# Kernel optimization log

Measured on AMD Instinct MI355X. Metric: run time of the kernel, lower is better.

Reference implementation:

```python
import jax, jax.numpy as jnp
import numpy as np

B, C, H, W = 16, 512, 32, 32
NUM_HEADS = 8
GROUPS = 32
EPS = 1e-5


def setup_inputs() -> dict:
    key = jax.random.key(0)
    ks = jax.random.split(key, 3)
    x = jax.random.normal(ks[0], (B, C, H, W), dtype=jnp.float32)
    # Conv2d 1x1 weights stored as (out, in); init ~ fan-in scaled normal
    qkv_w = jax.random.normal(ks[1], (3 * C, C), dtype=jnp.float32) * (C ** -0.5)
    proj_w = jax.random.normal(ks[2], (C, C), dtype=jnp.float32) * (C ** -0.5)
    return {
        "x": x,
        "norm_w": jnp.ones((C,), jnp.float32),
        "norm_b": jnp.zeros((C,), jnp.float32),
        "qkv_w": qkv_w,
        "qkv_b": jnp.zeros((3 * C,), jnp.float32),
        "proj_w": proj_w,
        "proj_b": jnp.zeros((C,), jnp.float32),
    }


def reference(x, norm_w, norm_b, qkv_w, qkv_b, proj_w, proj_b):
    b, c, hh, ww = x.shape
    nh = NUM_HEADS
    hd = c // nh
    n = hh * ww

    # GroupNorm(32, C)
    xg = x.reshape(b, GROUPS, c // GROUPS, hh, ww)
    mean = xg.mean(axis=(2, 3, 4), keepdims=True)
    var = ((xg - mean) ** 2).mean(axis=(2, 3, 4), keepdims=True)
    hn = ((xg - mean) * jax.lax.rsqrt(var + EPS)).reshape(b, c, hh, ww)
    hn = hn * norm_w[None, :, None, None] + norm_b[None, :, None, None]

    # 1x1 conv QKV projection
    qkv = jnp.einsum('bchw,oc->bohw', hn, qkv_w) + qkv_b[None, :, None, None]
    # (B,3C,H,W) -> (B,3,nh,hd,N) -> (3,B,nh,N,hd)
    qkv = qkv.reshape(b, 3, nh, hd, n).transpose(1, 0, 2, 4, 3)
    q, k, v = qkv[0], qkv[1], qkv[2]

    scale = hd ** -0.5
    attn = jax.nn.softmax(jnp.einsum('bhnd,bhmd->bhnm', q, k) * scale, axis=-1)
    o = jnp.einsum('bhnm,bhmd->bhnd', attn, v)  # (B,nh,N,hd)
    o = o.transpose(0, 1, 3, 2).reshape(b, c, hh, ww)

    out = jnp.einsum('bchw,oc->bohw', o, proj_w) + proj_b[None, :, None, None]
    return out + x
```

## Files before the change

### kernel.cpp

```cpp
#include <hip/hip_runtime.h>
#include <cstdint>
#include <math.h>


typedef __bf16 bf16;
typedef __attribute__((ext_vector_type(8))) __bf16 bf16x8;
typedef __attribute__((ext_vector_type(4))) float f32x4;
typedef __attribute__((ext_vector_type(4))) short s16x4;

union U8 { uint4 u4; bf16x8 v; bf16 h[8]; };
union U4 { ushort4 u; bf16 h[4]; };
union UB4 { ushort4 u; s16x4 s; bf16 h[4]; };
union F4 { float4 v; float f[4]; };

typedef __attribute__((address_space(1))) void* gp1;
typedef __attribute__((address_space(3))) void* lp3;

__device__ __forceinline__ void async16(const void* g, void* l) {
  __builtin_amdgcn_global_load_lds((gp1)g, (lp3)l, 16, 0, 0);
}

#define LOG2E 1.44269504f

__global__ __launch_bounds__(256) void cvt_w(const float* __restrict__ qw,
                                             const float* __restrict__ pw,
                                             bf16* __restrict__ qwb,
                                             bf16* __restrict__ pwb) {
  int i = blockIdx.x * 256 + threadIdx.x;
  F4 v; bf16* dst;
  if (i < 196608) { v.v = ((const float4*)qw)[i]; dst = qwb + (size_t)i * 4; }
  else { v.v = ((const float4*)pw)[i - 196608]; dst = pwb + (size_t)(i - 196608) * 4; }
  U4 o;
#pragma unroll
  for (int j = 0; j < 4; j++) o.h[j] = (bf16)v.f[j];
  *(ushort4*)dst = o.u;
}

__global__ __launch_bounds__(256) void gn_stats(const float* __restrict__ x,
                                                float2* __restrict__ stats) {
  int bg = blockIdx.x;
  const float* base = x + (size_t)bg * 16384;
  int t = threadIdx.x;
  float s = 0.f, ss = 0.f;
#pragma unroll
  for (int p = 0; p < 16; p++) {
    F4 u; u.v = *(const float4*)(base + (size_t)(p * 256 + t) * 4);
#pragma unroll
    for (int i = 0; i < 4; i++) { float v = u.f[i]; s += v; ss += v * v; }
  }
  for (int off = 1; off < 64; off <<= 1) { s += __shfl_xor(s, off); ss += __shfl_xor(ss, off); }
  __shared__ float red[8];
  int w = t >> 6;
  if ((t & 63) == 0) { red[w] = s; red[4 + w] = ss; }
  __syncthreads();
  if (t == 0) {
    float S = red[0] + red[1] + red[2] + red[3];
    float SS = red[4] + red[5] + red[6] + red[7];
    float mean = S * (1.f / 16384.f);
    float var = SS * (1.f / 16384.f) - mean * mean;
    stats[bg] = make_float2(mean, rsqrtf(var + 1e-5f));
  }
}

__global__ __launch_bounds__(256) void gn_apply(const float* __restrict__ x,
                                                const float* __restrict__ nwp,
                                                const float* __restrict__ nbp,
                                                const float2* __restrict__ stats,
                                                bf16* __restrict__ hnt) {
  int b = blockIdx.z, nt = blockIdx.y, ct = blockIdx.x;
  int t = threadIdx.x, w = t >> 6, l = t & 63;
  int wc = w & 1, wn = w >> 1;
  int cb = ct * 128 + wc * 64 + (l & 7) * 8;
  int n0 = nt * 64 + wn * 32 + (l >> 3) * 4;
  float2 ms = stats[b * 32 + (cb >> 4)];
  float wgt[8], bia[8];
#pragma unroll
  for (int i = 0; i < 8; i++) {
    float wi = nwp[cb + i] * ms.y;
    wgt[i] = wi;
    bia[i] = nbp[cb + i] - ms.x * wi;
  }
  F4 in[8];
  const float* xb = x + ((size_t)b * 512 + cb) * 1024 + n0;
#pragma unroll
  for (int i = 0; i < 8; i++) in[i].v = *(const float4*)(xb + (size_t)i * 1024);
  bf16* ob = hnt + ((size_t)b * 1024 + n0) * 512 + cb;
#pragma unroll
  for (int j = 0; j < 4; j++) {
    U8 o;
#pragma unroll
    for (int i = 0; i < 8; i++) o.h[i] = (bf16)(in[i].f[j] * wgt[i] + bia[i]);
    *(uint4*)(ob + (size_t)j * 512) = o.u4;
  }
}

__device__ __forceinline__ void gemm_bt_core(const bf16* ga0, const bf16* gb0,
                                             bf16* At, bf16* Bt,
                                             f32x4 (&acc)[4][4], int w, int l) {
  const bf16* ga = ga0 + (size_t)(w * 16 + (l >> 2)) * 512 + (l & 3) * 8;
  const bf16* gb = gb0 + (size_t)(w * 16 + (l >> 2)) * 512 + (l & 3) * 8;
  int wr = w >> 1, wc = w & 1;
  const bf16* Ab = At + (wr * 64 + (l & 15)) * 32 + (l >> 4) * 8;
  const bf16* Bb = Bt + (wc * 64 + (l & 15)) * 32 + (l >> 4) * 8;
  bf16* lA = At + w * 16 * 32;
  bf16* lB = Bt + w * 16 * 32;
  for (int k0 = 0; k0 < 512; k0 += 32) {
    async16(ga + k0, lA);
    async16(ga + 64 * 512 + k0, lA + 64 * 32);
    async16(gb + k0, lB);
    async16(gb + 64 * 512 + k0, lB + 64 * 32);
    __syncthreads();
    bf16x8 af[4], bfr[4];
#pragma unroll
    for (int i = 0; i < 4; i++) {
      af[i] = *(const bf16x8*)(Ab + i * 512);
      bfr[i] = *(const bf16x8*)(Bb + i * 512);
    }
#pragma unroll
    for (int i = 0; i < 4; i++)
#pragma unroll
      for (int j = 0; j < 4; j++)
        acc[i][j] = __builtin_amdgcn_mfma_f32_16x16x32_bf16(af[i], bfr[j], acc[i][j], 0, 0, 0);
    __syncthreads();
  }
}

__global__ __launch_bounds__(256, 2) void qkv_gemm(const bf16* __restrict__ hnt,
                                                   const bf16* __restrict__ qwb,
                                                   const float* __restrict__ qb,
                                                   bf16* __restrict__ qsw,
                                                   bf16* __restrict__ ksw,
                                                   bf16* __restrict__ vsw) {
  __shared__ bf16 At[128 * 32];
  __shared__ bf16 Bt[128 * 32];
  int b = blockIdx.z, mt = blockIdx.y, ot = blockIdx.x;
  int m0 = mt * 128, o0 = ot * 128;
  int t = threadIdx.x, w = t >> 6, l = t & 63;
  f32x4 acc[4][4] = {};
  gemm_bt_core(hnt + ((size_t)b * 1024 + m0) * 512, qwb + (size_t)o0 * 512, At, Bt, acc, w, l);

  int wr = w >> 1, wc = w & 1, quad = l >> 4, li = l & 15;
#pragma unroll
  for (int i = 0; i < 4; i++) {
    int gnb = m0 + wr * 64 + i * 16;
    int blk = gnb >> 4;
#pragma unroll
    for (int j = 0; j < 4; j++) {
      int go = o0 + wc * 64 + j * 16 + li;
      float bias = qb[go];
      if (ot < 8) {
        int c = (ot < 4) ? go : (go - 512);
        int hh = c >> 6, d = c & 63;
        int ks = d >> 5, dq = (d >> 3) & 3, jj = d & 7;
        bf16* base = ((ot < 4) ? qsw : ksw) + ((size_t)(b * 8 + hh) << 16)
                     + (blk * 2 + ks) * 512 + dq * 8 + jj;
#pragma unroll
        for (int r = 0; r < 4; r++)
          base[(quad * 4 + r) * 32] = (bf16)(acc[i][j][r] + bias);
      } else {
        int c = go - 1024;
        int hh = c >> 6, d = c & 63;
        int df = d >> 4, lv = d & 15;
        bf16* base = vsw + ((size_t)(b * 8 + hh) << 16)
                     + (blk * 4 + df) * 256 + (lv * 4 + quad) * 4;
        U4 pk;
#pragma unroll
        for (int r = 0; r < 4; r++) pk.h[r] = (bf16)(acc[i][j][r] + bias);
        *(ushort4*)base = pk.u;
      }
    }
  }
}

__global__ __launch_bounds__(256, 4) void attn(const bf16* __restrict__ qsw,
                                               const bf16* __restrict__ ksw,
                                               const bf16* __restrict__ vsw,
                                               bf16* __restrict__ ont) {
  int bh = blockIdx.x;
  int b = bh >> 3, h = bh & 7;
  int qt = blockIdx.y;
  int t = threadIdx.x, w = t >> 6, l = t & 63;
  int quad = l >> 4, li = l & 15;
  int q0 = qt * 128 + w * 32;

  int laneK = (li * 4 + quad) * 8;
  int laneV = (li * 4 + quad) * 4;
  const bf16* qp = qsw + ((size_t)bh << 16) + laneK;
  const bf16* kp = ksw + ((size_t)bh << 16) + laneK;
  const bf16* vp = vsw + ((size_t)bh << 16) + laneV;

  const float QS = 0.125f * LOG2E;
  bf16x8 qfr[2][2];
#pragma unroll
  for (int qf = 0; qf < 2; qf++)
#pragma unroll
    for (int ks = 0; ks < 2; ks++) {
      U8 u;
      u.u4 = *(const uint4*)(qp + (((q0 >> 4) + qf) * 2 + ks) * 512);
#pragma unroll
      for (int i = 0; i < 8; i++) u.h[i] = (bf16)((float)u.h[i] * QS);
      qfr[qf][ks] = u.v;
    }

  float mrun[2] = {-INFINITY, -INFINITY}, lrun[2] = {0.f, 0.f};
  f32x4 of[4][2] = {};

  U8 ka[2], kc[2];
#pragma unroll
  for (int kf = 0; kf < 2; kf++) {
    ka[kf].u4 = *(const uint4*)(kp + kf * 1024);
    kc[kf].u4 = *(const uint4*)(kp + kf * 1024 + 512);
  }

  for (int c = 0; c < 32; c++) {
    int cb = c * 2048;
    UB4 va[2][4];
#pragma unroll
    for (int kf = 0; kf < 2; kf++)
#pragma unroll
      for (int df = 0; df < 4; df++)
        va[kf][df].u = *(const ushort4*)(vp + cb + kf * 1024 + df * 256);
    f32x4 st[2][2] = {};
#pragma unroll
    for (int kf = 0; kf < 2; kf++) {
      st[0][kf] = __builtin_amdgcn_mfma_f32_16x16x32_bf16(ka[kf].v, qfr[0][0], st[0][kf], 0, 0, 0);
      st[1][kf] = __builtin_amdgcn_mfma_f32_16x16x32_bf16(ka[kf].v, qfr[1][0], st[1][kf], 0, 0, 0);
      st[0][kf] = __builtin_amdgcn_mfma_f32_16x16x32_bf16(kc[kf].v, qfr[0][1], st[0][kf], 0, 0, 0);
      st[1][kf] = __builtin_amdgcn_mfma_f32_16x16x32_bf16(kc[kf].v, qfr[1][1], st[1][kf], 0, 0, 0);
    }
    int cn = ((c + 1) & 31) * 2048;
    U8 nka[2], nkc[2];
#pragma unroll
    for (int kf = 0; kf < 2; kf++) {
      nka[kf].u4 = *(const uint4*)(kp + cn + kf * 1024);
      nkc[kf].u4 = *(const uint4*)(kp + cn + kf * 1024 + 512);
    }
    UB4 pfr[2][2];
#pragma unroll
    for (int qf = 0; qf < 2; qf++) {
      f32x4 vm = st[qf][0];
#pragma unroll
      for (int r = 0; r < 4; r++) vm[r] = fmaxf(vm[r], st[qf][1][r]);
      float mt = fmaxf(fmaxf(vm[0], vm[1]), fmaxf(vm[2], vm[3]));
      mt = fmaxf(mt, __shfl_xor(mt, 16));
      mt = fmaxf(mt, __shfl_xor(mt, 32));
      float mold = mrun[qf];
      float mnew = fmaxf(mold, mt);
      mrun[qf] = mnew;
      f32x4 vs = {};
#pragma unroll
      for (int kf = 0; kf < 2; kf++)
#pragma unroll
        for (int r = 0; r < 4; r++) {
          float e = __builtin_amdgcn_exp2f(st[qf][kf][r] - mnew);
          vs[r] += e;
          pfr[qf][kf].h[r] = (bf16)e;
        }
      float ls = (vs[0] + vs[1]) + (vs[2] + vs[3]);
      ls += __shfl_xor(ls, 16);
      ls += __shfl_xor(ls, 32);
      if (__ballot(mnew > mold)) {
        float alpha = __builtin_amdgcn_exp2f(mold - mnew);
        lrun[qf] = lrun[qf] * alpha + ls;
#pragma unroll
        for (int df = 0; df < 4; df++)
#pragma unroll
          for (int r = 0; r < 4; r++) of[df][qf][r] *= alpha;
      } else {
        lrun[qf] += ls;
      }
    }
#pragma unroll
    for (int kf = 0; kf < 2; kf++)
#pragma unroll
      for (int df = 0; df < 4; df++)
#pragma unroll
        for (int qf = 0; qf < 2; qf++)
          of[df][qf] = __builtin_amdgcn_mfma_f32_16x16x16bf16_1k(va[kf][df].s, pfr[qf][kf].s, of[df][qf], 0, 0, 0);
#pragma unroll
    for (int kf = 0; kf < 2; kf++) { ka[kf] = nka[kf]; kc[kf] = nkc[kf]; }
  }
#pragma unroll
  for (int qf = 0; qf < 2; qf++) {
    float inv = 1.f / lrun[qf];
    bf16* ob = ont + ((size_t)b * 1024 + q0 + qf * 16 + li) * 512 + h * 64 + quad * 4;
#pragma unroll
    for (int df = 0; df < 4; df++) {
      U4 pk;
#pragma unroll
      for (int r = 0; r < 4; r++) pk.h[r] = (bf16)(of[df][qf][r] * inv);
      *(ushort4*)(ob + df * 16) = pk.u;
    }
  }
}

__global__ __launch_bounds__(256, 2) void proj_gemm(const bf16* __restrict__ ont,
                                                    const bf16* __restrict__ pwb,
                                                    const float* __restrict__ pb,
                                                    const float* __restrict__ x,
                                                    float* __restrict__ out) {
  __shared__ bf16 At[128 * 32];
  __shared__ bf16 Bt[128 * 32];
  int b = blockIdx.z, mt = blockIdx.y, ot = blockIdx.x;
  int m0 = mt * 128, o0 = ot * 128;
  int t = threadIdx.x, w = t >> 6, l = t & 63;
  f32x4 acc[4][4] = {};
  gemm_bt_core(ont + ((size_t)b * 1024 + m0) * 512, pwb + (size_t)o0 * 512, At, Bt, acc, w, l);

  int wr = w >> 1, wc = w & 1, quad = l >> 4, li = l & 15;
#pragma unroll
  for (int i = 0; i < 4; i++) {
    int gn = m0 + wr * 64 + i * 16 + quad * 4;
#pragma unroll
    for (int j = 0; j < 4; j++) {
      int go = o0 + wc * 64 + j * 16 + li;
      float bias = pb[go];
      F4 xres; xres.v = *(const float4*)(x + ((size_t)b * 512 + go) * 1024 + gn);
      F4 o;
#pragma unroll
      for (int r = 0; r < 4; r++) o.f[r] = acc[i][j][r] + bias + xres.f[r];
      *(float4*)(out + ((size_t)b * 512 + go) * 1024 + gn) = o.v;
    }
  }
}

extern "C" void kernel_launch(void* const* d_in, const int* in_sizes, int n_in,
                              void* d_out, int out_size, void* d_ws, size_t ws_size,
                              hipStream_t stream) {
  const float* x  = (const float*)d_in[0];
  const float* nw = (const float*)d_in[1];
  const float* nb = (const float*)d_in[2];
  const float* qw = (const float*)d_in[3];
  const float* qb = (const float*)d_in[4];
  const float* pw = (const float*)d_in[5];
  const float* pb = (const float*)d_in[6];
  float* out = (float*)d_out;

  char* ws = (char*)d_ws;
  float2* stats = (float2*)ws;
  bf16* qwb = (bf16*)(ws + (64u << 10));
  bf16* pwb = (bf16*)(ws + (2u << 20));
  bf16* hnt = (bf16*)(ws + (4u << 20));
  bf16* qsw = (bf16*)(ws + (20u << 20));
  bf16* ksw = (bf16*)(ws + (36u << 20));
  bf16* vsw = (bf16*)(ws + (52u << 20));
  bf16* ont = hnt;

  cvt_w<<<1024, 256, 0, stream>>>(qw, pw, qwb, pwb);
  gn_stats<<<512, 256, 0, stream>>>(x, stats);
  gn_apply<<<dim3(4, 16, 16), 256, 0, stream>>>(x, nw, nb, stats, hnt);
  qkv_gemm<<<dim3(12, 8, 16), 256, 0, stream>>>(hnt, qwb, qb, qsw, ksw, vsw);
  attn<<<dim3(128, 8, 1), 256, 0, stream>>>(qsw, ksw, vsw, ont);
  proj_gemm<<<dim3(4, 8, 16), 256, 0, stream>>>(ont, pwb, pb, x, out);
}
```

Measured before the change: 231.2 us.

## Use lazy max rescaling and deferred row-sum reduction in attention loop

The attention inner loop now rescales the running max only when a tile's max exceeds the current max by more than 8 (in log2 units), skipping the cross-lane max shuffles otherwise. Row sums are kept as per-lane partial vectors and reduced across lanes once at the end instead of every iteration. The loop is manually unrolled by two with ping-pong K register buffers, removing the copies, and s_setprio raises wave priority around the MFMA blocks. The lazy threshold lets exp2 values reach up to 2^8 before rescaling, which relies on fp32 and bf16 range to stay accurate.

Measured after the change: 238.3 us. 3.1% more time.

```diff
diff --git a/kernel.cpp b/kernel.cpp
--- a/kernel.cpp
+++ b/kernel.cpp
@@ -172,6 +172,77 @@
   }
 }
 
+__device__ __forceinline__ void attn_body(const bf16* __restrict__ kp,
+                                          const bf16* __restrict__ vp, int c,
+                                          U8 (&ka)[2], U8 (&kc)[2],
+                                          U8 (&nka)[2], U8 (&nkc)[2],
+                                          const bf16x8 (&qfr)[2][2],
+                                          float (&mrun)[2], f32x4 (&lacc)[2],
+                                          f32x4 (&of)[4][2]) {
+  int cb = c * 2048;
+  UB4 va[2][4];
+#pragma unroll
+  for (int kf = 0; kf < 2; kf++)
+#pragma unroll
+    for (int df = 0; df < 4; df++)
+      va[kf][df].u = *(const ushort4*)(vp + cb + kf * 1024 + df * 256);
+  f32x4 st[2][2] = {};
+  __builtin_amdgcn_s_setprio(1);
+#pragma unroll
+  for (int kf = 0; kf < 2; kf++) {
+    st[0][kf] = __builtin_amdgcn_mfma_f32_16x16x32_bf16(ka[kf].v, qfr[0][0], st[0][kf], 0, 0, 0);
+    st[1][kf] = __builtin_amdgcn_mfma_f32_16x16x32_bf16(ka[kf].v, qfr[1][0], st[1][kf], 0, 0, 0);
+    st[0][kf] = __builtin_amdgcn_mfma_f32_16x16x32_bf16(kc[kf].v, qfr[0][1], st[0][kf], 0, 0, 0);
+    st[1][kf] = __builtin_amdgcn_mfma_f32_16x16x32_bf16(kc[kf].v, qfr[1][1], st[1][kf], 0, 0, 0);
+  }
+  __builtin_amdgcn_s_setprio(0);
+  int cn = ((c + 1) & 31) * 2048;
+#pragma unroll
+  for (int kf = 0; kf < 2; kf++) {
+    nka[kf].u4 = *(const uint4*)(kp + cn + kf * 1024);
+    nkc[kf].u4 = *(const uint4*)(kp + cn + kf * 1024 + 512);
+  }
+  UB4 pfr[2][2];
+#pragma unroll
+  for (int qf = 0; qf < 2; qf++) {
+    float mt = fmaxf(fmaxf(fmaxf(st[qf][0][0], st[qf][0][1]),
+                           fmaxf(st[qf][0][2], st[qf][0][3])),
+                     fmaxf(fmaxf(st[qf][1][0], st[qf][1][1]),
+                           fmaxf(st[qf][1][2], st[qf][1][3])));
+    if (__ballot(mt > mrun[qf] + 8.f)) {
+      mt = fmaxf(mt, __shfl_xor(mt, 16));
+      mt = fmaxf(mt, __shfl_xor(mt, 32));
+      float mnew = fmaxf(mrun[qf], mt);
+      float alpha = __builtin_amdgcn_exp2f(mrun[qf] - mnew);
+      mrun[qf] = mnew;
+#pragma unroll
+      for (int r = 0; r < 4; r++) lacc[qf][r] *= alpha;
+#pragma unroll
+      for (int df = 0; df < 4; df++)
+#pragma unroll
+        for (int r = 0; r < 4; r++) of[df][qf][r] *= alpha;
+    }
+    float m = mrun[qf];
+#pragma unroll
+    for (int kf = 0; kf < 2; kf++)
+#pragma unroll
+      for (int r = 0; r < 4; r++) {
+        float e = __builtin_amdgcn_exp2f(st[qf][kf][r] - m);
+        lacc[qf][r] += e;
+        pfr[qf][kf].h[r] = (bf16)e;
+      }
+  }
+  __builtin_amdgcn_s_setprio(1);
+#pragma unroll
+  for (int kf = 0; kf < 2; kf++)
+#pragma unroll
+    for (int df = 0; df < 4; df++)
+#pragma unroll
+      for (int qf = 0; qf < 2; qf++)
+        of[df][qf] = __builtin_amdgcn_mfma_f32_16x16x16bf16_1k(va[kf][df].s, pfr[qf][kf].s, of[df][qf], 0, 0, 0);
+  __builtin_amdgcn_s_setprio(0);
+}
+
 __global__ __launch_bounds__(256, 4) void attn(const bf16* __restrict__ qsw,
                                                const bf16* __restrict__ ksw,
                                                const bf16* __restrict__ vsw,
@@ -202,87 +273,28 @@
       qfr[qf][ks] = u.v;
     }
 
-  float mrun[2] = {-INFINITY, -INFINITY}, lrun[2] = {0.f, 0.f};
+  float mrun[2] = {-INFINITY, -INFINITY};
+  f32x4 lacc[2] = {};
   f32x4 of[4][2] = {};
 
-  U8 ka[2], kc[2];
+  U8 ka0[2], kc0[2], ka1[2], kc1[2];
 #pragma unroll
   for (int kf = 0; kf < 2; kf++) {
-    ka[kf].u4 = *(const uint4*)(kp + kf * 1024);
-    kc[kf].u4 = *(const uint4*)(kp + kf * 1024 + 512);
-  }
-
-  for (int c = 0; c < 32; c++) {
-    int cb = c * 2048;
-    UB4 va[2][4];
-#pragma unroll
-    for (int kf = 0; kf < 2; kf++)
-#pragma unroll
-      for (int df = 0; df < 4; df++)
-        va[kf][df].u = *(const ushort4*)(vp + cb + kf * 1024 + df * 256);
-    f32x4 st[2][2] = {};
-#pragma unroll
-    for (int kf = 0; kf < 2; kf++) {
-      st[0][kf] = __builtin_amdgcn_mfma_f32_16x16x32_bf16(ka[kf].v, qfr[0][0], st[0][kf], 0, 0, 0);
-      st[1][kf] = __builtin_amdgcn_mfma_f32_16x16x32_bf16(ka[kf].v, qfr[1][0], st[1][kf], 0, 0, 0);
-      st[0][kf] = __builtin_amdgcn_mfma_f32_16x16x32_bf16(kc[kf].v, qfr[0][1], st[0][kf], 0, 0, 0);
-      st[1][kf] = __builtin_amdgcn_mfma_f32_16x16x32_bf16(kc[kf].v, qfr[1][1], st[1][kf], 0, 0, 0);
-    }
-    int cn = ((c + 1) & 31) * 2048;
-    U8 nka[2], nkc[2];
-#pragma unroll
-    for (int kf = 0; kf < 2; kf++) {
-      nka[kf].u4 = *(const uint4*)(kp + cn + kf * 1024);
-      nkc[kf].u4 = *(const uint4*)(kp + cn + kf * 1024 + 512);
-    }
-    UB4 pfr[2][2];
-#pragma unroll
-    for (int qf = 0; qf < 2; qf++) {
-      f32x4 vm = st[qf][0];
-#pragma unroll
-      for (int r = 0; r < 4; r++) vm[r] = fmaxf(vm[r], st[qf][1][r]);
-      float mt = fmaxf(fmaxf(vm[0], vm[1]), fmaxf(vm[2], vm[3]));
-      mt = fmaxf(mt, __shfl_xor(mt, 16));
-      mt = fmaxf(mt, __shfl_xor(mt, 32));
-      float mold = mrun[qf];
-      float mnew = fmaxf(mold, mt);
-      mrun[qf] = mnew;
-      f32x4 vs = {};
-#pragma unroll
-      for (int kf = 0; kf < 2; kf++)
-#pragma unroll
-        for (int r = 0; r < 4; r++) {
-          float e = __builtin_amdgcn_exp2f(st[qf][kf][r] - mnew);
-          vs[r] += e;
-          pfr[qf][kf].h[r] = (bf16)e;
-        }
-      float ls = (vs[0] + vs[1]) + (vs[2] + vs[3]);
-      ls += __shfl_xor(ls, 16);
-      ls += __shfl_xor(ls, 32);
-      if (__ballot(mnew > mold)) {
-        float alpha = __builtin_amdgcn_exp2f(mold - mnew);
-        lrun[qf] = lrun[qf] * alpha + ls;
-#pragma unroll
-        for (int df = 0; df < 4; df++)
-#pragma unroll
-          for (int r = 0; r < 4; r++) of[df][qf][r] *= alpha;
-      } else {
-        lrun[qf] += ls;
-      }
-    }
-#pragma unroll
-    for (int kf = 0; kf < 2; kf++)
-#pragma unroll
-      for (int df = 0; df < 4; df++)
-#pragma unroll
-        for (int qf = 0; qf < 2; qf++)
-          of[df][qf] = __builtin_amdgcn_mfma_f32_16x16x16bf16_1k(va[kf][df].s, pfr[qf][kf].s, of[df][qf], 0, 0, 0);
-#pragma unroll
-    for (int kf = 0; kf < 2; kf++) { ka[kf] = nka[kf]; kc[kf] = nkc[kf]; }
-  }
+    ka0[kf].u4 = *(const uint4*)(kp + kf * 1024);
+    kc0[kf].u4 = *(const uint4*)(kp + kf * 1024 + 512);
+  }
+
+  for (int c = 0; c < 32; c += 2) {
+    attn_body(kp, vp, c,     ka0, kc0, ka1, kc1, qfr, mrun, lacc, of);
+    attn_body(kp, vp, c + 1, ka1, kc1, ka0, kc0, qfr, mrun, lacc, of);
+  }
+
 #pragma unroll
   for (int qf = 0; qf < 2; qf++) {
-    float inv = 1.f / lrun[qf];
+    float lsum = (lacc[qf][0] + lacc[qf][1]) + (lacc[qf][2] + lacc[qf][3]);
+    lsum += __shfl_xor(lsum, 16);
+    lsum += __shfl_xor(lsum, 32);
+    float inv = 1.f / lsum;
     bf16* ob = ont + ((size_t)b * 1024 + q0 + qf * 16 + li) * 512 + h * 64 + quad * 4;
 #pragma unroll
     for (int df = 0; df < 4; df++) {
```
